# Performance work log

Hardware: AMD Instinct MI355X
Metric: run time of the kernel (lower is better)

The kernel has to match this reference:

```python
import jax, jax.numpy as jnp
import numpy as np

C = 512
B, H, W = 4, 64, 64
GROUPS = 32
EPS = 1e-6
SCALE = 1.0 / np.sqrt(C)


def setup_inputs() -> dict:
    key = jax.random.key(0)
    ks = jax.random.split(key, 3)
    x = jax.random.normal(ks[0], (B, C, H, W), dtype=jnp.float32)
    # conv weights: kaiming-ish small init for numerical sanity
    qkv_w = jax.random.normal(ks[1], (3 * C, C), dtype=jnp.float32) * (1.0 / np.sqrt(C))
    proj_w = jax.random.normal(ks[2], (C, C), dtype=jnp.float32) * (1.0 / np.sqrt(C))
    return {
        "x": x,
        "norm_w": jnp.ones((C,), jnp.float32),
        "norm_b": jnp.zeros((C,), jnp.float32),
        "qkv_w": qkv_w,
        "qkv_b": jnp.zeros((3 * C,), jnp.float32),
        "proj_w": proj_w,
        "proj_b": jnp.zeros((C,), jnp.float32),
    }


def reference(x, norm_w, norm_b, qkv_w, qkv_b, proj_w, proj_b):
    b, c, h, w = x.shape
    hw = h * w
    # GroupNorm(32, eps=1e-6, affine)
    xg = x.reshape(b, GROUPS, -1)                       # [B, G, (C/G)*H*W]
    mean = jnp.mean(xg, axis=-1, keepdims=True)
    var = jnp.var(xg, axis=-1, keepdims=True)
    xn = ((xg - mean) * jax.lax.rsqrt(var + EPS)).reshape(b, c, h, w)
    xn = xn * norm_w[:, None, None] + norm_b[:, None, None]
    # 1x1 conv qkv == channel matmul
    qkv = jnp.einsum('oc,bchw->bohw', qkv_w, xn) + qkv_b[:, None, None]
    q, k, v = jnp.split(qkv, 3, axis=1)                 # each [B, C, H, W]
    q = q.reshape(b, c, hw)                              # [B, C, HW]
    k = k.reshape(b, c, hw)
    v = v.reshape(b, c, hw)
    # attn[b, i, j] = softmax_j( q_i . k_j * scale )
    scores = jnp.einsum('bci,bcj->bij', q, k) * SCALE    # [B, HW, HW]
    attn = jax.nn.softmax(scores, axis=-1)
    # h[b, c, i] = sum_j v[b, c, j] * attn[b, i, j]
    hmap = jnp.einsum('bcj,bij->bci', v, attn).reshape(b, c, h, w)
    out = x + jnp.einsum('oc,bchw->bohw', proj_w, hmap) + proj_b[:, None, None]
    return out
```

## Files before the change

### kernel.cpp

```cpp
#include <hip/hip_runtime.h>
#include <hip/hip_fp8.h>
#include <cstdint>
#include <cmath>

#define B_   4
#define C_   512
#define HW_  4096
#define G_   32
#define CPG_ 16
#define EPS_ 1e-6f
#define SCALE_ 0.04419417382415922f
#define PSCALE_ 0.0625f


typedef __bf16 bf16_t;
typedef __bf16 bf16x8 __attribute__((ext_vector_type(8)));
typedef float  f32x4  __attribute__((ext_vector_type(4)));
typedef int    i32x4  __attribute__((ext_vector_type(4)));
typedef int    i32x8  __attribute__((ext_vector_type(8)));
typedef unsigned int u32;
typedef __hip_fp8_e4m3 fp8_t;

__device__ __forceinline__ void cp16(const void* g, void* l) {
  __builtin_amdgcn_global_load_lds((__attribute__((address_space(1))) u32*)(g),
                                   (__attribute__((address_space(3))) u32*)(l),
                                   16, 0, 0);
}

__device__ __forceinline__ void zero_acc(f32x4 acc[4][4]) {
  f32x4 z = {0.f, 0.f, 0.f, 0.f};
#pragma unroll
  for (int i = 0; i < 4; ++i)
#pragma unroll
    for (int j = 0; j < 4; ++j) acc[i][j] = z;
}

template <bool ROWSUM, int SA = 0x7F, int SB = 0x7F>
__device__ __forceinline__ void gemm_bt_mx(const unsigned char* __restrict__ A,
                                           const unsigned char* __restrict__ B,
                                           int K, int lda, int ldb,
                                           f32x4 acc[4][4], f32x4 accl[4]) {
  __shared__ __align__(16) unsigned char As[128 * 128];
  __shared__ __align__(16) unsigned char Bs[128 * 128];
  const int tid  = threadIdx.x;
  const int wave = tid >> 6;
  const int lane = tid & 63;
  const int wm = (wave >> 1) * 64;
  const int wn = (wave & 1) * 64;
  const int srow = lane >> 3;
  const int gch  = ((lane & 7) - srow) & 7;
  const unsigned char* gA = A + (size_t)(wave * 32 + srow) * lda + gch * 16;
  const unsigned char* gB = B + (size_t)(wave * 32 + srow) * ldb + gch * 16;
  unsigned char* lA = As + wave * 32 * 128;
  unsigned char* lB = Bs + wave * 32 * 128;
  const int fr = lane & 15;
  const int q  = lane >> 4;
  const int co0 = ((2 * q     + fr) & 7) * 16;
  const int co1 = ((2 * q + 1 + fr) & 7) * 16;
  const i32x8 vones = {0x38383838, 0x38383838, 0x38383838, 0x38383838,
                       0x38383838, 0x38383838, 0x38383838, 0x38383838};

  for (int k0 = 0; k0 < K; k0 += 128) {
#pragma unroll
    for (int cc = 0; cc < 4; ++cc) {
      cp16(gA + (size_t)(cc * 8) * lda, lA + cc * 1024);
      cp16(gB + (size_t)(cc * 8) * ldb, lB + cc * 1024);
    }
    gA += 128; gB += 128;
    __syncthreads();
    i32x8 a[4], b[4];
#pragma unroll
    for (int i = 0; i < 4; ++i) {
      const int ro = (wm + i * 16 + fr) * 128;
      i32x4 lo = *(const i32x4*)(As + ro + co0);
      i32x4 hi = *(const i32x4*)(As + ro + co1);
      a[i] = __builtin_shufflevector(lo, hi, 0, 1, 2, 3, 4, 5, 6, 7);
    }
#pragma unroll
    for (int j = 0; j < 4; ++j) {
      const int ro = (wn + j * 16 + fr) * 128;
      i32x4 lo = *(const i32x4*)(Bs + ro + co0);
      i32x4 hi = *(const i32x4*)(Bs + ro + co1);
      b[j] = __builtin_shufflevector(lo, hi, 0, 1, 2, 3, 4, 5, 6, 7);
    }
#pragma unroll
    for (int i = 0; i < 4; ++i) {
#pragma unroll
      for (int j = 0; j < 4; ++j)
        acc[i][j] = __builtin_amdgcn_mfma_scale_f32_16x16x128_f8f6f4(
            a[i], b[j], acc[i][j], 0, 0, 0, SA, 0, SB);
      if (ROWSUM)
        accl[i] = __builtin_amdgcn_mfma_scale_f32_16x16x128_f8f6f4(
            a[i], vones, accl[i], 0, 0, 0, SA, 0, 0x7F);
    }
    __syncthreads();
  }
}


__global__ void __launch_bounds__(256) cast_w_kernel(const float* __restrict__ qkv_w,
                                                     const float* __restrict__ proj_w,
                                                     fp8_t* __restrict__ wqkv8,
                                                     fp8_t* __restrict__ wproj8) {
  const int idx = blockIdx.x * 256 + threadIdx.x;
  const int t = idx * 4;
  const int nq = 1536 * 512;
  if (t < nq) {
    u32 dw = 0;
    dw = (u32)__builtin_amdgcn_cvt_pk_fp8_f32(qkv_w[t] * 16.f, qkv_w[t + 1] * 16.f, (int)dw, false);
    dw = (u32)__builtin_amdgcn_cvt_pk_fp8_f32(qkv_w[t + 2] * 16.f, qkv_w[t + 3] * 16.f, (int)dw, true);
    *(u32*)((unsigned char*)wqkv8 + t) = dw;
  } else {
    const int tt = t - nq;
    const int o = tt >> 9;
    const int p = tt & 511;
    float v[4];
#pragma unroll
    for (int e = 0; e < 4; ++e) {
      const int pe = p + e;
      const int off = pe & 63;
      const int c = (pe & ~63) + ((off & 3) << 4) + (off >> 2);
      v[e] = proj_w[(o << 9) + c] * 16.f;
    }
    u32 dw = 0;
    dw = (u32)__builtin_amdgcn_cvt_pk_fp8_f32(v[0], v[1], (int)dw, false);
    dw = (u32)__builtin_amdgcn_cvt_pk_fp8_f32(v[2], v[3], (int)dw, true);
    *(u32*)((unsigned char*)wproj8 + tt) = dw;
  }
}

__global__ void __launch_bounds__(256) gn_partial_kernel(const float* __restrict__ x,
                                                         float* __restrict__ stats) {
  __shared__ float rs[256], rss[256];
  const int bg = blockIdx.x >> 3;
  const int ch = blockIdx.x & 7;
  const float4* base = (const float4*)(x + (size_t)bg * (CPG_ * HW_)) +
                       (size_t)ch * (CPG_ * HW_ / 4 / 8);
  float s = 0.f, ss = 0.f;
  for (int i = threadIdx.x; i < CPG_ * HW_ / 4 / 8; i += 256) {
    float4 v = base[i];
    s  += v.x + v.y + v.z + v.w;
    ss += v.x * v.x + v.y * v.y + v.z * v.z + v.w * v.w;
  }
  rs[threadIdx.x] = s; rss[threadIdx.x] = ss;
  __syncthreads();
  for (int st = 128; st > 0; st >>= 1) {
    if ((int)threadIdx.x < st) {
      rs[threadIdx.x]  += rs[threadIdx.x + st];
      rss[threadIdx.x] += rss[threadIdx.x + st];
    }
    __syncthreads();
  }
  if (threadIdx.x == 0) {
    atomicAdd(&stats[bg * 2 + 0], rs[0]);
    atomicAdd(&stats[bg * 2 + 1], rss[0]);
  }
}

__global__ void __launch_bounds__(256) norm_tr_kernel(const float* __restrict__ x,
                                                      const float* __restrict__ stats,
                                                      const float* __restrict__ nw,
                                                      const float* __restrict__ nb,
                                                      fp8_t* __restrict__ xnT8) {
  __shared__ float tile[64][65];
  const int b  = blockIdx.z;
  const int i0 = blockIdx.x * 64;
  const int c0 = blockIdx.y * 64;
  const int tx = threadIdx.x & 63;
  const int ty = threadIdx.x >> 6;
  const int cbase = c0 + ty * 16;
  const int g = cbase >> 4;
  const float inv = 1.f / (float)(CPG_ * HW_);
  const float sum  = stats[(b * G_ + g) * 2 + 0];
  const float ssum = stats[(b * G_ + g) * 2 + 1];
  const float mean = sum * inv;
  const float rstd = rsqrtf(ssum * inv - mean * mean + EPS_);
#pragma unroll
  for (int r = 0; r < 16; ++r) {
    const int c = cbase + r;
    float v = x[((size_t)b * C_ + c) * HW_ + i0 + tx];
    tile[ty * 16 + r][tx] = (v - mean) * rstd * nw[c] + nb[c];
  }
  __syncthreads();
  const int il = threadIdx.x >> 2;
  const int q4 = threadIdx.x & 3;
#pragma unroll
  for (int m = 0; m < 4; ++m) {
    const int cq = q4 + m * 4;
    u32 dw = 0;
    dw = (u32)__builtin_amdgcn_cvt_pk_fp8_f32(tile[cq * 4 + 0][il], tile[cq * 4 + 1][il], (int)dw, false);
    dw = (u32)__builtin_amdgcn_cvt_pk_fp8_f32(tile[cq * 4 + 2][il], tile[cq * 4 + 3][il], (int)dw, true);
    *(u32*)((unsigned char*)xnT8 + ((size_t)b * HW_ + i0 + il) * C_ + c0 + cq * 4) = dw;
  }
}


__global__ void __launch_bounds__(256) qk_gemm_kernel(const fp8_t* __restrict__ xnT8,
                                                      const fp8_t* __restrict__ wqkv8,
                                                      const float* __restrict__ qkv_b,
                                                      fp8_t* __restrict__ QKt8) {
  const int b = blockIdx.z;
  f32x4 acc[4][4]; zero_acc(acc);
  const unsigned char* A  = (const unsigned char*)xnT8 + ((size_t)b * HW_ + blockIdx.y * 128) * C_;
  const unsigned char* Bp = (const unsigned char*)wqkv8 + (size_t)blockIdx.x * 128 * C_;
  gemm_bt_mx<false, 0x7F, 0x7B>(A, Bp, C_, C_, C_, acc, nullptr);
  const int lane = threadIdx.x & 63, wave = threadIdx.x >> 6;
  const int wm = (wave >> 1) * 64, wn = (wave & 1) * 64;
  const int fr = lane & 15, q = lane >> 4;
  const int r0 = blockIdx.y * 128 + wm + (q << 2);
  const int cb = blockIdx.x * 128 + wn;
  float bias[4];
#pragma unroll
  for (int j = 0; j < 4; ++j) bias[j] = qkv_b[cb + fr + j * 16];
#pragma unroll
  for (int i = 0; i < 4; ++i)
#pragma unroll
    for (int r = 0; r < 4; ++r) {
      const int row = r0 + i * 16 + r;
      u32 dw = 0;
      dw = (u32)__builtin_amdgcn_cvt_pk_fp8_f32(acc[i][0][r] + bias[0],
                                                acc[i][1][r] + bias[1], (int)dw, false);
      dw = (u32)__builtin_amdgcn_cvt_pk_fp8_f32(acc[i][2][r] + bias[2],
                                                acc[i][3][r] + bias[3], (int)dw, true);
      *(u32*)((unsigned char*)QKt8 + ((size_t)b * HW_ + row) * 1024 + cb + fr * 4) = dw;
    }
}

__global__ void __launch_bounds__(256) v_gemm_kernel(const fp8_t* __restrict__ wqkv8,
                                                     const fp8_t* __restrict__ xnT8,
                                                     const float* __restrict__ qkv_b,
                                                     fp8_t* __restrict__ V8) {
  const int b = blockIdx.z;
  f32x4 acc[4][4]; zero_acc(acc);
  const unsigned char* A  = (const unsigned char*)wqkv8 + (size_t)(1024 + blockIdx.y * 128) * C_;
  const unsigned char* Bp = (const unsigned char*)xnT8 + ((size_t)b * HW_ + blockIdx.x * 128) * C_;
  gemm_bt_mx<false, 0x7B, 0x7F>(A, Bp, C_, C_, C_, acc, nullptr);
  const int lane = threadIdx.x & 63, wave = threadIdx.x >> 6;
  const int wm = (wave >> 1) * 64, wn = (wave & 1) * 64;
  const int fr = lane & 15, q = lane >> 4;
  const int r0 = blockIdx.y * 128 + wm + (q << 2);
  const int cb = blockIdx.x * 128 + wn;
#pragma unroll
  for (int i = 0; i < 4; ++i)
#pragma unroll
    for (int r = 0; r < 4; ++r) {
      const int row = r0 + i * 16 + r;
      const float bias = qkv_b[1024 + row];
      u32 dw = 0;
      dw = (u32)__builtin_amdgcn_cvt_pk_fp8_f32(acc[i][0][r] + bias,
                                                acc[i][1][r] + bias, (int)dw, false);
      dw = (u32)__builtin_amdgcn_cvt_pk_fp8_f32(acc[i][2][r] + bias,
                                                acc[i][3][r] + bias, (int)dw, true);
      *(u32*)((unsigned char*)V8 + ((size_t)b * C_ + row) * HW_ + cb + fr * 4) = dw;
    }
}

__global__ void __launch_bounds__(256) sexp_gemm_kernel(const fp8_t* __restrict__ QKt8,
                                                        fp8_t* __restrict__ P8) {
  const int n   = blockIdx.x;
  const int xcd = n & 7;
  const int p   = n >> 3;
  const int xb  = p & 31;
  const int grp = xcd * 16 + (p >> 5);
  const int yb  = grp & 31;
  const int b   = grp >> 5;

  const unsigned char* QKtb = (const unsigned char*)QKt8 + (size_t)b * HW_ * 1024;
  fp8_t* Pb = P8 + (size_t)b * HW_ * HW_;
  f32x4 acc[4][4]; zero_acc(acc);
  const unsigned char* A  = QKtb + (size_t)yb * 128 * 1024;
  const unsigned char* Bp = QKtb + 512 + (size_t)xb * 128 * 1024;
  gemm_bt_mx<false>(A, Bp, 512, 1024, 1024, acc, nullptr);
  const int lane = threadIdx.x & 63, wave = threadIdx.x >> 6;
  const int wm = (wave >> 1) * 64, wn = (wave & 1) * 64;
  const int fr = lane & 15, q = lane >> 4;
  const int r0 = yb * 128 + wm + (q << 2);
  const int cb = xb * 128 + wn;
#pragma unroll
  for (int i = 0; i < 4; ++i)
#pragma unroll
    for (int r = 0; r < 4; ++r) {
      const int row = r0 + i * 16 + r;
      float e0 = __expf(acc[i][0][r] * SCALE_) * PSCALE_;
      float e1 = __expf(acc[i][1][r] * SCALE_) * PSCALE_;
      float e2 = __expf(acc[i][2][r] * SCALE_) * PSCALE_;
      float e3 = __expf(acc[i][3][r] * SCALE_) * PSCALE_;
      u32 dw = 0;
      dw = (u32)__builtin_amdgcn_cvt_pk_fp8_f32(e0, e1, (int)dw, false);
      dw = (u32)__builtin_amdgcn_cvt_pk_fp8_f32(e2, e3, (int)dw, true);
      *(u32*)((unsigned char*)Pb + (size_t)row * HW_ + cb + fr * 4) = dw;
    }
}

__global__ void __launch_bounds__(256) pv_gemm_kernel(const fp8_t* __restrict__ P8,
                                                      const fp8_t* __restrict__ V8,
                                                      fp8_t* __restrict__ hmT8) {
  const int n   = blockIdx.x;
  const int xcd = n & 7;
  const int p   = n >> 3;
  const int xb  = p & 3;
  const int grp = xcd * 16 + (p >> 2);
  const int yb  = grp & 31;
  const int b   = grp >> 5;

  const unsigned char* A  = (const unsigned char*)P8 + (size_t)b * HW_ * HW_ +
                            (size_t)yb * 128 * HW_;
  const unsigned char* Bp = (const unsigned char*)V8 + (size_t)b * C_ * HW_ +
                            (size_t)xb * 128 * HW_;
  fp8_t* hmTb = hmT8 + (size_t)b * HW_ * C_;

  f32x4 acc[4][4]; zero_acc(acc);
  f32x4 accl[4];
  {
    f32x4 z = {0.f, 0.f, 0.f, 0.f};
#pragma unroll
    for (int i = 0; i < 4; ++i) accl[i] = z;
  }
  gemm_bt_mx<true>(A, Bp, HW_, HW_, HW_, acc, accl);

  const int lane = threadIdx.x & 63, wave = threadIdx.x >> 6;
  const int wm = (wave >> 1) * 64, wn = (wave & 1) * 64;
  const int fr = lane & 15, q = lane >> 4;
  const int r0 = yb * 128 + wm + (q << 2);
  const int cb = xb * 128 + wn;
#pragma unroll
  for (int i = 0; i < 4; ++i)
#pragma unroll
    for (int r = 0; r < 4; ++r) {
      const int row = r0 + i * 16 + r;
      const float rl = 16.f / accl[i][r];
      u32 dw = 0;
      dw = (u32)__builtin_amdgcn_cvt_pk_fp8_f32(acc[i][0][r] * rl, acc[i][1][r] * rl, (int)dw, false);
      dw = (u32)__builtin_amdgcn_cvt_pk_fp8_f32(acc[i][2][r] * rl, acc[i][3][r] * rl, (int)dw, true);
      *(u32*)((unsigned char*)hmTb + (size_t)row * C_ + cb + fr * 4) = dw;
    }
}

__global__ void __launch_bounds__(256) proj_gemm_kernel(const fp8_t* __restrict__ wproj8,
                                                        const fp8_t* __restrict__ hmT8,
                                                        const float* __restrict__ proj_b,
                                                        const float* __restrict__ x,
                                                        float* __restrict__ out) {
  const int b = blockIdx.z;
  f32x4 acc[4][4]; zero_acc(acc);
  const unsigned char* A  = (const unsigned char*)wproj8 + (size_t)blockIdx.y * 128 * C_;
  const unsigned char* Bp = (const unsigned char*)hmT8 + ((size_t)b * HW_ + blockIdx.x * 128) * C_;
  gemm_bt_mx<false, 0x7B, 0x7B>(A, Bp, C_, C_, C_, acc, nullptr);
  const int lane = threadIdx.x & 63, wave = threadIdx.x >> 6;
  const int wm = (wave >> 1) * 64, wn = (wave & 1) * 64;
  const int r0 = blockIdx.y * 128 + wm + ((lane >> 4) << 2);
  const int c0 = blockIdx.x * 128 + wn + (lane & 15);
#pragma unroll
  for (int i = 0; i < 4; ++i)
#pragma unroll
    for (int r = 0; r < 4; ++r) {
      const int row = r0 + i * 16 + r;
      const float bias = proj_b[row];
#pragma unroll
      for (int j = 0; j < 4; ++j) {
        const int col = c0 + j * 16;
        const size_t idx = ((size_t)b * C_ + row) * HW_ + col;
        out[idx] = x[idx] + bias + acc[i][j][r];
      }
    }
}

extern "C" void kernel_launch(void* const* d_in, const int* in_sizes, int n_in,
                              void* d_out, int out_size, void* d_ws, size_t ws_size,
                              hipStream_t stream) {
  const float* x      = (const float*)d_in[0];
  const float* norm_w = (const float*)d_in[1];
  const float* norm_b = (const float*)d_in[2];
  const float* qkv_w  = (const float*)d_in[3];
  const float* qkv_b  = (const float*)d_in[4];
  const float* proj_w = (const float*)d_in[5];
  const float* proj_b = (const float*)d_in[6];
  float* out = (float*)d_out;

  char* ws = (char*)d_ws;
  size_t o = 0;
  fp8_t* wqkv8  = (fp8_t*)(ws + o); o += (size_t)1536 * 512;
  fp8_t* wproj8 = (fp8_t*)(ws + o); o += (size_t)512 * 512;
  float* stats  = (float*)(ws + o); o += 128 * 2 * 4;
  fp8_t* xnT8   = (fp8_t*)(ws + o); o += (size_t)B_ * HW_ * C_;
  fp8_t* QKt8   = (fp8_t*)(ws + o); o += (size_t)B_ * HW_ * 1024;
  fp8_t* V8     = (fp8_t*)(ws + o); o += (size_t)B_ * C_ * HW_;
  fp8_t* hmT8   = (fp8_t*)(ws + o); o += (size_t)B_ * HW_ * C_;
  fp8_t* P8     = (fp8_t*)(ws + o); o += (size_t)B_ * HW_ * HW_;

  cast_w_kernel<<<1024, 256, 0, stream>>>(qkv_w, proj_w, wqkv8, wproj8);
  hipMemsetAsync(stats, 0, 128 * 2 * sizeof(float), stream);
  gn_partial_kernel<<<1024, 256, 0, stream>>>(x, stats);
  norm_tr_kernel<<<dim3(HW_ / 64, C_ / 64, B_), 256, 0, stream>>>(x, stats, norm_w, norm_b, xnT8);
  qk_gemm_kernel<<<dim3(1024 / 128, HW_ / 128, B_), 256, 0, stream>>>(xnT8, wqkv8, qkv_b, QKt8);
  v_gemm_kernel<<<dim3(HW_ / 128, C_ / 128, B_), 256, 0, stream>>>(wqkv8, xnT8, qkv_b, V8);
  sexp_gemm_kernel<<<4096, 256, 0, stream>>>(QKt8, P8);
  pv_gemm_kernel<<<512, 256, 0, stream>>>(P8, V8, hmT8);
  proj_gemm_kernel<<<dim3(HW_ / 128, C_ / 128, B_), 256, 0, stream>>>(
      wproj8, hmT8, proj_b, x, out);
}
```

Baseline: 238.3 us.

## Fuse score-exp and PV GEMMs into a single flash-style attention kernel

Replaces the separate exp-score GEMM (which wrote a full B*HW*HW fp8 probability matrix to global memory) and the PV GEMM with one fused kernel. Each block keeps a 64-row Q panel in registers, streams K tiles through double-buffered LDS, computes exp scores, stages them in LDS, and multiplies them immediately against V loaded from global memory. The row sum is accumulated with an MFMA against a ones vector. This removes the 64MB P round trip and one launch, but it runs only 256 blocks of 512 threads with large LDS use, so occupancy is limited and V is re-read by every panel.

```diff
diff --git a/kernel.cpp b/kernel.cpp
--- a/kernel.cpp
+++ b/kernel.cpp
@@ -255,84 +255,198 @@
     }
 }
 
-__global__ void __launch_bounds__(256) sexp_gemm_kernel(const fp8_t* __restrict__ QKt8,
-                                                        fp8_t* __restrict__ P8) {
-  const int n   = blockIdx.x;
-  const int xcd = n & 7;
-  const int p   = n >> 3;
-  const int xb  = p & 31;
-  const int grp = xcd * 16 + (p >> 5);
-  const int yb  = grp & 31;
-  const int b   = grp >> 5;
-
-  const unsigned char* QKtb = (const unsigned char*)QKt8 + (size_t)b * HW_ * 1024;
-  fp8_t* Pb = P8 + (size_t)b * HW_ * HW_;
-  f32x4 acc[4][4]; zero_acc(acc);
-  const unsigned char* A  = QKtb + (size_t)yb * 128 * 1024;
-  const unsigned char* Bp = QKtb + 512 + (size_t)xb * 128 * 1024;
-  gemm_bt_mx<false>(A, Bp, 512, 1024, 1024, acc, nullptr);
-  const int lane = threadIdx.x & 63, wave = threadIdx.x >> 6;
-  const int wm = (wave >> 1) * 64, wn = (wave & 1) * 64;
-  const int fr = lane & 15, q = lane >> 4;
-  const int r0 = yb * 128 + wm + (q << 2);
-  const int cb = xb * 128 + wn;
-#pragma unroll
-  for (int i = 0; i < 4; ++i)
-#pragma unroll
-    for (int r = 0; r < 4; ++r) {
-      const int row = r0 + i * 16 + r;
-      float e0 = __expf(acc[i][0][r] * SCALE_) * PSCALE_;
-      float e1 = __expf(acc[i][1][r] * SCALE_) * PSCALE_;
-      float e2 = __expf(acc[i][2][r] * SCALE_) * PSCALE_;
-      float e3 = __expf(acc[i][3][r] * SCALE_) * PSCALE_;
-      u32 dw = 0;
-      dw = (u32)__builtin_amdgcn_cvt_pk_fp8_f32(e0, e1, (int)dw, false);
-      dw = (u32)__builtin_amdgcn_cvt_pk_fp8_f32(e2, e3, (int)dw, true);
-      *(u32*)((unsigned char*)Pb + (size_t)row * HW_ + cb + fr * 4) = dw;
-    }
-}
-
-__global__ void __launch_bounds__(256) pv_gemm_kernel(const fp8_t* __restrict__ P8,
-                                                      const fp8_t* __restrict__ V8,
-                                                      fp8_t* __restrict__ hmT8) {
-  const int n   = blockIdx.x;
-  const int xcd = n & 7;
-  const int p   = n >> 3;
-  const int xb  = p & 3;
-  const int grp = xcd * 16 + (p >> 2);
-  const int yb  = grp & 31;
-  const int b   = grp >> 5;
-
-  const unsigned char* A  = (const unsigned char*)P8 + (size_t)b * HW_ * HW_ +
-                            (size_t)yb * 128 * HW_;
-  const unsigned char* Bp = (const unsigned char*)V8 + (size_t)b * C_ * HW_ +
-                            (size_t)xb * 128 * HW_;
-  fp8_t* hmTb = hmT8 + (size_t)b * HW_ * C_;
-
-  f32x4 acc[4][4]; zero_acc(acc);
-  f32x4 accl[4];
+__global__ void __launch_bounds__(512, 2)
+fused_attn_kernel(const fp8_t* __restrict__ QKt8, const fp8_t* __restrict__ V8,
+                  fp8_t* __restrict__ hmT8) {
+  __shared__ __align__(16) unsigned char lds[2 * 65536 + 8192];
+  unsigned char* plds = lds + 131072;
+
+  const int n     = blockIdx.x;
+  const int xcd   = n & 7;
+  const int b     = xcd >> 1;
+  const int panel = (xcd & 1) * 32 + (n >> 3);
+
+  const int tid  = threadIdx.x;
+  const int lane = tid & 63;
+  const int wave = tid >> 6;
+  const int fr   = lane & 15;
+  const int q    = lane >> 4;
+  const int ih   = wave & 1;
+  const int jq   = wave >> 1;
+  const int cg   = wave >> 1;
+
+  const unsigned char* QKb = (const unsigned char*)QKt8 + (size_t)b * HW_ * 1024;
+  const unsigned char* gK  = QKb + 512;
+
+  const int sch = tid & 31;
+  const int srw = tid >> 5;
+
+#pragma unroll
+  for (int p = 0; p < 4; ++p) {
+    const int row = p * 16 + srw;
+    cp16(QKb + (size_t)(panel * 64 + row) * 1024 + (((sch - row) & 31) << 4),
+         lds + 65536 + row * 512 + sch * 16);
+  }
+  asm volatile("s_waitcnt vmcnt(0)" ::: "memory");
+  __builtin_amdgcn_s_barrier();
+
+  i32x8 qf[2][4];
+#pragma unroll
+  for (int ii = 0; ii < 2; ++ii) {
+    const int row = ih * 32 + ii * 16 + fr;
+    const unsigned char* qr = lds + 65536 + row * 512;
+#pragma unroll
+    for (int k = 0; k < 4; ++k) {
+      i32x4 lo = *(const i32x4*)(qr + (((k * 8 + 2 * q + row) & 31) << 4));
+      i32x4 hi = *(const i32x4*)(qr + (((k * 8 + 2 * q + 1 + row) & 31) << 4));
+      qf[ii][k] = __builtin_shufflevector(lo, hi, 0, 1, 2, 3, 4, 5, 6, 7);
+    }
+  }
+  asm volatile("s_waitcnt lgkmcnt(0)" ::: "memory");
+  __builtin_amdgcn_s_barrier();
+
+#pragma unroll
+  for (int p = 0; p < 8; ++p) {
+    const int row = p * 16 + srw;
+    cp16(gK + (size_t)row * 1024 + (((sch - row) & 31) << 4),
+         lds + row * 512 + sch * 16);
+  }
+
+  f32x4 pvacc[2][8];
   {
     f32x4 z = {0.f, 0.f, 0.f, 0.f};
 #pragma unroll
-    for (int i = 0; i < 4; ++i) accl[i] = z;
-  }
-  gemm_bt_mx<true>(A, Bp, HW_, HW_, HW_, acc, accl);
-
-  const int lane = threadIdx.x & 63, wave = threadIdx.x >> 6;
-  const int wm = (wave >> 1) * 64, wn = (wave & 1) * 64;
-  const int fr = lane & 15, q = lane >> 4;
-  const int r0 = yb * 128 + wm + (q << 2);
-  const int cb = xb * 128 + wn;
-#pragma unroll
-  for (int i = 0; i < 4; ++i)
+    for (int i = 0; i < 2; ++i)
+#pragma unroll
+      for (int j = 0; j < 8; ++j) pvacc[i][j] = z;
+  }
+  f32x4 accl[2];
+  {
+    f32x4 z = {0.f, 0.f, 0.f, 0.f};
+    accl[0] = z; accl[1] = z;
+  }
+  const i32x8 vones = {0x38383838, 0x38383838, 0x38383838, 0x38383838,
+                       0x38383838, 0x38383838, 0x38383838, 0x38383838};
+
+  const unsigned char* vbase = (const unsigned char*)V8 +
+      ((size_t)b * C_ + cg * 128 + fr) * HW_ + q * 32;
+
+  unsigned char* cur = lds;
+  unsigned char* nxt = lds + 65536;
+
+  const int kr0 = jq * 32 + fr;
+  const int kr1 = kr0 + 16;
+  const int offb = (jq >> 1) * 64 + fr * 4 + (jq & 1) * 2;
+
+#pragma unroll 1
+  for (int t = 0; t < 32; ++t) {
+    if (t < 31) {
+#pragma unroll
+      for (int p = 0; p < 8; ++p) {
+        const int row = p * 16 + srw;
+        cp16(gK + (size_t)((t + 1) * 128 + row) * 1024 + (((sch - row) & 31) << 4),
+             nxt + row * 512 + sch * 16);
+      }
+      asm volatile("s_waitcnt vmcnt(8)" ::: "memory");
+    } else {
+      asm volatile("s_waitcnt vmcnt(0)" ::: "memory");
+    }
+    __builtin_amdgcn_s_barrier();
+
+    f32x4 sacc[2][2];
+    {
+      f32x4 z = {0.f, 0.f, 0.f, 0.f};
+      sacc[0][0] = z; sacc[0][1] = z; sacc[1][0] = z; sacc[1][1] = z;
+    }
+    const unsigned char* k0p = cur + kr0 * 512;
+    const unsigned char* k1p = cur + kr1 * 512;
+#pragma unroll
+    for (int k = 0; k < 4; ++k) {
+      i32x4 l0 = *(const i32x4*)(k0p + (((k * 8 + 2 * q + kr0) & 31) << 4));
+      i32x4 h0 = *(const i32x4*)(k0p + (((k * 8 + 2 * q + 1 + kr0) & 31) << 4));
+      i32x4 l1 = *(const i32x4*)(k1p + (((k * 8 + 2 * q + kr1) & 31) << 4));
+      i32x4 h1 = *(const i32x4*)(k1p + (((k * 8 + 2 * q + 1 + kr1) & 31) << 4));
+      i32x8 kf0 = __builtin_shufflevector(l0, h0, 0, 1, 2, 3, 4, 5, 6, 7);
+      i32x8 kf1 = __builtin_shufflevector(l1, h1, 0, 1, 2, 3, 4, 5, 6, 7);
+#pragma unroll
+      for (int ii = 0; ii < 2; ++ii) {
+        sacc[ii][0] = __builtin_amdgcn_mfma_scale_f32_16x16x128_f8f6f4(
+            qf[ii][k], kf0, sacc[ii][0], 0, 0, 0, 0x7F, 0, 0x7F);
+        sacc[ii][1] = __builtin_amdgcn_mfma_scale_f32_16x16x128_f8f6f4(
+            qf[ii][k], kf1, sacc[ii][1], 0, 0, 0, 0x7F, 0, 0x7F);
+      }
+    }
+
+#pragma unroll
+    for (int ii = 0; ii < 2; ++ii)
+#pragma unroll
+      for (int r = 0; r < 4; ++r) {
+        const int row = ih * 32 + ii * 16 + q * 4 + r;
+        float e0 = __expf(sacc[ii][0][r] * SCALE_) * PSCALE_;
+        float e1 = __expf(sacc[ii][1][r] * SCALE_) * PSCALE_;
+        u32 dw = (u32)__builtin_amdgcn_cvt_pk_fp8_f32(e0, e1, 0, false);
+        *(unsigned short*)(plds + row * 128 + ((((offb >> 4) + row) & 7) << 4) +
+                           (offb & 15)) = (unsigned short)dw;
+      }
+
+    const unsigned char* vp = vbase + t * 128;
+    i32x4 vl[8], vh[8];
+#pragma unroll
+    for (int c = 0; c < 3; ++c) {
+      vl[c] = *(const i32x4*)(vp + (size_t)(c * 16) * HW_);
+      vh[c] = *(const i32x4*)(vp + (size_t)(c * 16) * HW_ + 16);
+    }
+
+    asm volatile("s_waitcnt lgkmcnt(0)" ::: "memory");
+    __builtin_amdgcn_s_barrier();
+
+    i32x8 pa[2];
+#pragma unroll
+    for (int ii = 0; ii < 2; ++ii) {
+      const int prow = ih * 32 + ii * 16 + fr;
+      const unsigned char* pp = plds + prow * 128;
+      i32x4 lo = *(const i32x4*)(pp + (((2 * q + prow) & 7) << 4));
+      i32x4 hi = *(const i32x4*)(pp + (((2 * q + 1 + prow) & 7) << 4));
+      pa[ii] = __builtin_shufflevector(lo, hi, 0, 1, 2, 3, 4, 5, 6, 7);
+    }
+    __builtin_amdgcn_s_setprio(1);
+#pragma unroll
+    for (int c = 0; c < 8; ++c) {
+      if (c < 5) {
+        vl[c + 3] = *(const i32x4*)(vp + (size_t)((c + 3) * 16) * HW_);
+        vh[c + 3] = *(const i32x4*)(vp + (size_t)((c + 3) * 16) * HW_ + 16);
+      }
+      i32x8 v = __builtin_shufflevector(vl[c], vh[c], 0, 1, 2, 3, 4, 5, 6, 7);
+      pvacc[0][c] = __builtin_amdgcn_mfma_scale_f32_16x16x128_f8f6f4(
+          pa[0], v, pvacc[0][c], 0, 0, 0, 0x7F, 0, 0x7F);
+      pvacc[1][c] = __builtin_amdgcn_mfma_scale_f32_16x16x128_f8f6f4(
+          pa[1], v, pvacc[1][c], 0, 0, 0, 0x7F, 0, 0x7F);
+    }
+    accl[0] = __builtin_amdgcn_mfma_scale_f32_16x16x128_f8f6f4(
+        pa[0], vones, accl[0], 0, 0, 0, 0x7F, 0, 0x7F);
+    accl[1] = __builtin_amdgcn_mfma_scale_f32_16x16x128_f8f6f4(
+        pa[1], vones, accl[1], 0, 0, 0, 0x7F, 0, 0x7F);
+    __builtin_amdgcn_s_setprio(0);
+
+    unsigned char* tmp = cur; cur = nxt; nxt = tmp;
+  }
+
+  unsigned char* hb = (unsigned char*)hmT8 + (size_t)b * HW_ * C_;
+#pragma unroll
+  for (int ii = 0; ii < 2; ++ii)
 #pragma unroll
     for (int r = 0; r < 4; ++r) {
-      const int row = r0 + i * 16 + r;
-      const float rl = 16.f / accl[i][r];
-      u32 dw = 0;
-      dw = (u32)__builtin_amdgcn_cvt_pk_fp8_f32(acc[i][0][r] * rl, acc[i][1][r] * rl, (int)dw, false);
-      dw = (u32)__builtin_amdgcn_cvt_pk_fp8_f32(acc[i][2][r] * rl, acc[i][3][r] * rl, (int)dw, true);
-      *(u32*)((unsigned char*)hmTb + (size_t)row * C_ + cb + fr * 4) = dw;
+      const int row = panel * 64 + ih * 32 + ii * 16 + q * 4 + r;
+      const float rl = 16.f / accl[ii][r];
+#pragma unroll
+      for (int g = 0; g < 2; ++g) {
+        u32 dw = 0;
+        dw = (u32)__builtin_amdgcn_cvt_pk_fp8_f32(pvacc[ii][g * 4 + 0][r] * rl,
+                                                  pvacc[ii][g * 4 + 1][r] * rl, (int)dw, false);
+        dw = (u32)__builtin_amdgcn_cvt_pk_fp8_f32(pvacc[ii][g * 4 + 2][r] * rl,
+                                                  pvacc[ii][g * 4 + 3][r] * rl, (int)dw, true);
+        *(u32*)(hb + (size_t)row * C_ + cg * 128 + g * 64 + fr * 4) = dw;
+      }
     }
 }
 
@@ -386,7 +500,6 @@
   fp8_t* QKt8   = (fp8_t*)(ws + o); o += (size_t)B_ * HW_ * 1024;
   fp8_t* V8     = (fp8_t*)(ws + o); o += (size_t)B_ * C_ * HW_;
   fp8_t* hmT8   = (fp8_t*)(ws + o); o += (size_t)B_ * HW_ * C_;
-  fp8_t* P8     = (fp8_t*)(ws + o); o += (size_t)B_ * HW_ * HW_;
 
   cast_w_kernel<<<1024, 256, 0, stream>>>(qkv_w, proj_w, wqkv8, wproj8);
   hipMemsetAsync(stats, 0, 128 * 2 * sizeof(float), stream);
@@ -394,8 +507,7 @@
   norm_tr_kernel<<<dim3(HW_ / 64, C_ / 64, B_), 256, 0, stream>>>(x, stats, norm_w, norm_b, xnT8);
   qk_gemm_kernel<<<dim3(1024 / 128, HW_ / 128, B_), 256, 0, stream>>>(xnT8, wqkv8, qkv_b, QKt8);
   v_gemm_kernel<<<dim3(HW_ / 128, C_ / 128, B_), 256, 0, stream>>>(wqkv8, xnT8, qkv_b, V8);
-  sexp_gemm_kernel<<<4096, 256, 0, stream>>>(QKt8, P8);
-  pv_gemm_kernel<<<512, 256, 0, stream>>>(P8, V8, hmT8);
+  fused_attn_kernel<<<256, 512, 0, stream>>>(QKt8, V8, hmT8);
   proj_gemm_kernel<<<dim3(HW_ / 128, C_ / 128, B_), 256, 0, stream>>>(
       wproj8, hmT8, proj_b, x, out);
 }
```

After: 309.5 us. 1.3x slower.

## Double-buffer LDS tiles in the FP8 MX GEMM to overlap loads with MFMA

Applied to the files above, without the earlier changes.

Gives the shared GEMM helper two LDS buffers per operand and prefetches the next K tile with global_load_lds while the current tile is consumed. Explicit vmcnt waits replace the full __syncthreads, and s_setprio raises wave priority around the MFMA block. This is meant to hide global-memory latency behind matrix math. In exchange LDS use per block doubles to 64KB, which can cut occupancy. Correctness also depends on the hand-counted vmcnt(8) matching the number of outstanding loads.

```diff
diff --git a/kernel.cpp b/kernel.cpp
--- a/kernel.cpp
+++ b/kernel.cpp
@@ -40,8 +40,8 @@
                                            const unsigned char* __restrict__ B,
                                            int K, int lda, int ldb,
                                            f32x4 acc[4][4], f32x4 accl[4]) {
-  __shared__ __align__(16) unsigned char As[128 * 128];
-  __shared__ __align__(16) unsigned char Bs[128 * 128];
+  __shared__ __align__(16) unsigned char As[2][128 * 128];
+  __shared__ __align__(16) unsigned char Bs[2][128 * 128];
   const int tid  = threadIdx.x;
   const int wave = tid >> 6;
   const int lane = tid & 63;
@@ -51,8 +51,7 @@
   const int gch  = ((lane & 7) - srow) & 7;
   const unsigned char* gA = A + (size_t)(wave * 32 + srow) * lda + gch * 16;
   const unsigned char* gB = B + (size_t)(wave * 32 + srow) * ldb + gch * 16;
-  unsigned char* lA = As + wave * 32 * 128;
-  unsigned char* lB = Bs + wave * 32 * 128;
+  const int lofs = wave * 32 * 128;
   const int fr = lane & 15;
   const int q  = lane >> 4;
   const int co0 = ((2 * q     + fr) & 7) * 16;
@@ -60,29 +59,48 @@
   const i32x8 vones = {0x38383838, 0x38383838, 0x38383838, 0x38383838,
                        0x38383838, 0x38383838, 0x38383838, 0x38383838};
 
-  for (int k0 = 0; k0 < K; k0 += 128) {
-#pragma unroll
-    for (int cc = 0; cc < 4; ++cc) {
-      cp16(gA + (size_t)(cc * 8) * lda, lA + cc * 1024);
-      cp16(gB + (size_t)(cc * 8) * ldb, lB + cc * 1024);
-    }
-    gA += 128; gB += 128;
-    __syncthreads();
+  const int nT = K >> 7;
+#pragma unroll
+  for (int cc = 0; cc < 4; ++cc) {
+    cp16(gA + (size_t)(cc * 8) * lda, &As[0][lofs + cc * 1024]);
+    cp16(gB + (size_t)(cc * 8) * ldb, &Bs[0][lofs + cc * 1024]);
+  }
+  gA += 128; gB += 128;
+
+#pragma unroll 1
+  for (int t = 0; t < nT; ++t) {
+    const int cur = t & 1;
+    if (t + 1 < nT) {
+#pragma unroll
+      for (int cc = 0; cc < 4; ++cc) {
+        cp16(gA + (size_t)(cc * 8) * lda, &As[cur ^ 1][lofs + cc * 1024]);
+        cp16(gB + (size_t)(cc * 8) * ldb, &Bs[cur ^ 1][lofs + cc * 1024]);
+      }
+      gA += 128; gB += 128;
+      asm volatile("s_waitcnt vmcnt(8)" ::: "memory");
+    } else {
+      asm volatile("s_waitcnt vmcnt(0)" ::: "memory");
+    }
+    __builtin_amdgcn_s_barrier();
+
     i32x8 a[4], b[4];
+    const unsigned char* Ab = As[cur];
+    const unsigned char* Bb = Bs[cur];
 #pragma unroll
     for (int i = 0; i < 4; ++i) {
       const int ro = (wm + i * 16 + fr) * 128;
-      i32x4 lo = *(const i32x4*)(As + ro + co0);
-      i32x4 hi = *(const i32x4*)(As + ro + co1);
+      i32x4 lo = *(const i32x4*)(Ab + ro + co0);
+      i32x4 hi = *(const i32x4*)(Ab + ro + co1);
       a[i] = __builtin_shufflevector(lo, hi, 0, 1, 2, 3, 4, 5, 6, 7);
     }
 #pragma unroll
     for (int j = 0; j < 4; ++j) {
       const int ro = (wn + j * 16 + fr) * 128;
-      i32x4 lo = *(const i32x4*)(Bs + ro + co0);
-      i32x4 hi = *(const i32x4*)(Bs + ro + co1);
+      i32x4 lo = *(const i32x4*)(Bb + ro + co0);
+      i32x4 hi = *(const i32x4*)(Bb + ro + co1);
       b[j] = __builtin_shufflevector(lo, hi, 0, 1, 2, 3, 4, 5, 6, 7);
     }
+    __builtin_amdgcn_s_setprio(1);
 #pragma unroll
     for (int i = 0; i < 4; ++i) {
 #pragma unroll
@@ -93,7 +111,8 @@
         accl[i] = __builtin_amdgcn_mfma_scale_f32_16x16x128_f8f6f4(
             a[i], vones, accl[i], 0, 0, 0, SA, 0, 0x7F);
     }
-    __syncthreads();
+    __builtin_amdgcn_s_setprio(0);
+    __builtin_amdgcn_s_barrier();
   }
 }
 
```

Result: no change. 235.6 us (-1.1%).
